# Kernel tuning notes

Measured on AMD Instinct MI355X. Metric: run time of the kernel, lower is better.

The kernel has to match this reference:

```python
import jax, jax.numpy as jnp
import numpy as np

EPS = 1e-5
SLOPE = 0.2  # leaky_relu negative_slope


def _mesh_conv_face(fe, gemm, w, b):
    # fe: [B, C, F]; gemm: [B, F, 3] neighbor face indices; w: [O, C, 4]; b: [O]
    # Gather 3 neighbor faces per face (irregular access).
    nb = jax.vmap(lambda f, g: f[:, g])(fe, gemm)  # [B, C, F, 3]
    n1, n2, n3 = nb[..., 0], nb[..., 1], nb[..., 2]
    # Symmetric (order-invariant) feature columns over the 3 neighbors.
    G = jnp.stack(
        [
            fe,                                                        # center face
            n1 + n2 + n3,                                              # sum
            jnp.abs(n1 - n2) + jnp.abs(n2 - n3) + jnp.abs(n3 - n1),    # pairwise abs-diff sum
            jnp.maximum(n1, jnp.maximum(n2, n3)),                      # max
        ],
        axis=-1,
    )  # [B, C, F, 4]
    # Conv2d with kernel (1,4) == contraction over (C, 4).
    return jnp.einsum('bcfk,ock->bof', G, w) + b[None, :, None]  # [B, O, F]


def _bn(x, gamma, beta):
    # BatchNorm2d (training mode) on [B, C, F]; normalize per-channel over (B, F).
    mu = x.mean(axis=(0, 2), keepdims=True)
    var = x.var(axis=(0, 2), keepdims=True)  # biased, as torch uses for normalization
    xn = (x - mu) * jax.lax.rsqrt(var + EPS)
    return gamma[None, :, None] * xn + beta[None, :, None]


def _lrelu(x):
    return jnp.where(x >= 0, x, SLOPE * x)


def setup_inputs() -> dict:
    key = jax.random.key(0)
    ks = jax.random.split(key, 8)
    B, Cin, Cout, F = 4, 32, 64, 50000
    fe = jax.random.normal(ks[0], (B, Cin, F), dtype=jnp.float32)
    gemm = jax.random.randint(ks[1], (B, F, 3), 0, F)
    w1 = jax.random.normal(ks[2], (Cout, Cin, 4), dtype=jnp.float32) * 0.05
    w2a = jax.random.normal(ks[3], (Cout, Cout, 4), dtype=jnp.float32) * 0.05
    w2b = jax.random.normal(ks[4], (Cout, Cout, 4), dtype=jnp.float32) * 0.05
    z = jnp.zeros((Cout,), jnp.float32)
    o = jnp.ones((Cout,), jnp.float32)
    return {
        'fe': fe, 'gemm': gemm,
        'w1': w1, 'b1': z, 'w2a': w2a, 'b2a': z, 'w2b': w2b, 'b2b': z,
        'g0': o, 'be0': z, 'g1': o, 'be1': z, 'g2': o, 'be2': z,
    }


def reference(fe, gemm, w1, b1, w2a, b2a, w2b, b2b, g0, be0, g1, be1, g2, be2):
    # conv1 -> BN -> LeakyReLU
    x1 = _lrelu(_bn(_mesh_conv_face(fe, gemm, w1, b1), g0, be0))
    # residual block 1
    x2 = _lrelu(_bn(_mesh_conv_face(x1, gemm, w2a, b2a), g1, be1) + x1)
    x1 = x2
    # residual block 2
    x2 = _lrelu(_bn(_mesh_conv_face(x1, gemm, w2b, b2b), g2, be2) + x1)
    return x2  # [B, Cout, F]; pool=0 so before_pool is None
```

## Files before the change

kernel.cpp:

```cpp
#include <hip/hip_runtime.h>
#include <hip/hip_bf16.h>
#include <math.h>


typedef __attribute__((ext_vector_type(8))) short short8;
typedef __attribute__((ext_vector_type(8))) unsigned short ushort8_t;
typedef __attribute__((ext_vector_type(4))) float f32x4;

__device__ inline unsigned short f2bf(float v) {
    union { float f; unsigned u; } x; x.f = v;
    unsigned r = x.u + 0x7fffu + ((x.u >> 16) & 1u);
    return (unsigned short)(r >> 16);
}
__device__ inline float bf2f(unsigned short u) {
    union { unsigned u; float f; } x; x.u = ((unsigned)u) << 16; return x.f;
}
__device__ inline unsigned pk2(float a, float b) {
    union { __hip_bfloat162 h; unsigned u; } c;
    c.h = __float22bfloat162_rn(make_float2(a, b));
    return c.u;
}

__global__ void transpose_fe_kernel(const float* __restrict__ fe,
                                    unsigned short* __restrict__ o, int F)
{
    __shared__ float tile[64 * 33];
    const int b = blockIdx.y;
    const int f0 = blockIdx.x * 64;
    const int t = threadIdx.x;
    const int lane = t & 63;
    const int w = t >> 6;
    const int f = f0 + lane;
    if (f < F) {
#pragma unroll
        for (int i = 0; i < 8; ++i) {
            const int c = w * 8 + i;
            tile[lane * 33 + c] = fe[((size_t)b * 32 + c) * F + f];
        }
    }
    __syncthreads();
    const int j = t >> 2, s = t & 3;
    const int fj = f0 + j;
    if (fj < F) {
        unsigned fw[4];
#pragma unroll
        for (int i = 0; i < 4; ++i)
            fw[i] = pk2(tile[j * 33 + s * 8 + 2 * i], tile[j * 33 + s * 8 + 2 * i + 1]);
        *(uint4*)(o + ((size_t)b * F + fj) * 32 + s * 8) = make_uint4(fw[0], fw[1], fw[2], fw[3]);
    }
}

__global__ void cast_weights_kernel(const float* __restrict__ w1,
                                    const float* __restrict__ w2a,
                                    const float* __restrict__ w2b,
                                    unsigned short* __restrict__ w1b,
                                    unsigned short* __restrict__ w2ab,
                                    unsigned short* __restrict__ w2bb)
{
    const int i = blockIdx.x * blockDim.x + threadIdx.x;
    if (i < 64 * 128) w1b[i] = f2bf(w1[i]);
    if (i < 64 * 256) { w2ab[i] = f2bf(w2a[i]); w2bb[i] = f2bf(w2b[i]); }
}

template <int CIN, bool NORM>
__launch_bounds__(256, (CIN == 32) ? 4 : 2)
__global__ void conv_mfma_kernel(const unsigned short* __restrict__ x,
                                 const int*   __restrict__ gidx,
                                 const unsigned short* __restrict__ wb,
                                 const float* __restrict__ bias,
                                 const float* __restrict__ mrIn,
                                 unsigned short* __restrict__ y,
                                 float* __restrict__ pS,
                                 float* __restrict__ pQ,
                                 int nb, int nbx, int F)
{
    constexpr int NSEG = CIN / 32;
    constexpr int K    = 4 * CIN;
    constexpr int RB   = 2 * K;
    constexpr int GB   = 64 * RB;
    constexpr int GREG = (GB > 17408) ? GB : 17408;
    __shared__ __align__(16) unsigned char smem[GREG + GB];
    float* tile = (float*)smem;
    unsigned char* Wb = smem + GREG;

    const int NBg = gridDim.x;
    const int t = threadIdx.x;
    const int j = t >> 2, s = t & 3;
    const int lane = t & 63, wv = t >> 6;
    const int l15 = lane & 15, quad = lane >> 4;
    const int kb = quad * 8;

    unsigned char* grow = smem + j * RB;
    const int swz = (j & 7) << 4;
    const int nrowi = wv * 16 + l15;
    const unsigned char* nrow = smem + nrowi * RB;
    const int nswz = (nrowi & 7) << 4;

#pragma unroll
    for (int u = 0; u < RB / 64; ++u) {
        const int qb = (s * (RB / 64) + u) * 16;
        const ushort8_t v = *(const ushort8_t*)(wb + (size_t)j * K + qb / 2);
        *(ushort8_t*)(Wb + j * RB + (qb ^ swz)) = v;
    }
    f32x4 bias4[4];
#pragma unroll
    for (int mt = 0; mt < 4; ++mt)
        bias4[mt] = *(const f32x4*)(bias + mt * 16 + quad * 4);

    float scr[NSEG * 8], shr[NSEG * 8];
    if constexpr (NORM) {
#pragma unroll
        for (int i = 0; i < NSEG; ++i) {
            const int c0 = (i * 4 + s) * 8;
#pragma unroll
            for (int h = 0; h < 2; ++h) {
                const f32x4 a  = *(const f32x4*)(mrIn + c0 + 4 * h);
                const f32x4 sh = *(const f32x4*)(mrIn + 64 + c0 + 4 * h);
#pragma unroll
                for (int q = 0; q < 4; ++q) {
                    scr[i * 8 + 4 * h + q] = a[q];
                    shr[i * 8 + 4 * h + q] = sh[q];
                }
            }
        }
    }

    ushort8_t vc[NSEG], v0[NSEG], v1[NSEG], v2[NSEG];
    int gA0, gA1, gA2;
    float S_acc = 0.f, Q_acc = 0.f;
    const int so = t & 63, sg = t >> 6;

    int tl = blockIdx.x;

    {
        const int b0 = tl / nbx;
        const int f0 = (tl - b0 * nbx) * 64;
        const int fc = min(f0 + j, F - 1);
        const int* gp = gidx + ((size_t)b0 * F + fc) * 3;
        const int g0 = gp[0], g1 = gp[1], g2 = gp[2];
        const unsigned short* xb = x + (size_t)b0 * F * CIN;
        const unsigned short* pc = xb + (size_t)fc * CIN;
        const unsigned short* p0 = xb + (size_t)g0 * CIN;
        const unsigned short* p1 = xb + (size_t)g1 * CIN;
        const unsigned short* p2 = xb + (size_t)g2 * CIN;
#pragma unroll
        for (int i = 0; i < NSEG; ++i) {
            const int c0 = (i * 4 + s) * 8;
            vc[i] = *(const ushort8_t*)(pc + c0);
            v0[i] = *(const ushort8_t*)(p0 + c0);
            v1[i] = *(const ushort8_t*)(p1 + c0);
            v2[i] = *(const ushort8_t*)(p2 + c0);
        }
    }
    {
        const int tn = min(tl + NBg, nb - 1);
        const int bn = tn / nbx;
        const int fn = min((tn - bn * nbx) * 64 + j, F - 1);
        const int* gp = gidx + ((size_t)bn * F + fn) * 3;
        gA0 = gp[0]; gA1 = gp[1]; gA2 = gp[2];
    }

    for (; tl < nb; tl += NBg) {
        const int b  = tl / nbx;
        const int f0 = (tl - b * nbx) * 64;

#pragma unroll
        for (int i = 0; i < NSEG; ++i) {
            const int c0 = (i * 4 + s) * 8;
            unsigned fw[16];
#pragma unroll
            for (int q = 0; q < 8; ++q) {
                float ctr = bf2f(vc[i][q]);
                float a   = bf2f(v0[i][q]);
                float bb  = bf2f(v1[i][q]);
                float cc  = bf2f(v2[i][q]);
                if constexpr (NORM) {
                    const float sc_ = scr[i * 8 + q], sh_ = shr[i * 8 + q];
                    ctr = fmaf(ctr, sc_, sh_); ctr = fmaxf(ctr, 0.2f * ctr);
                    a   = fmaf(a,   sc_, sh_); a   = fmaxf(a,   0.2f * a);
                    bb  = fmaf(bb,  sc_, sh_); bb  = fmaxf(bb,  0.2f * bb);
                    cc  = fmaf(cc,  sc_, sh_); cc  = fmaxf(cc,  0.2f * cc);
                }
                const float su = a + bb + cc;
                const float dd = fabsf(a - bb) + fabsf(bb - cc) + fabsf(cc - a);
                const float mm = fmaxf(a, fmaxf(bb, cc));
                fw[2 * q]     = pk2(ctr, su);
                fw[2 * q + 1] = pk2(dd, mm);
            }
#pragma unroll
            for (int q4 = 0; q4 < 4; ++q4) {
                const int qb = 8 * c0 + 16 * q4;
                *(uint4*)(grow + (qb ^ swz)) =
                    make_uint4(fw[4 * q4], fw[4 * q4 + 1], fw[4 * q4 + 2], fw[4 * q4 + 3]);
            }
        }

        {
            const int tn = min(tl + NBg, nb - 1);
            const int bn = tn / nbx;
            const int fcn = min((tn - bn * nbx) * 64 + j, F - 1);
            const unsigned short* xb = x + (size_t)bn * F * CIN;
            const unsigned short* pc = xb + (size_t)fcn * CIN;
            const unsigned short* p0 = xb + (size_t)gA0 * CIN;
            const unsigned short* p1 = xb + (size_t)gA1 * CIN;
            const unsigned short* p2 = xb + (size_t)gA2 * CIN;
#pragma unroll
            for (int i = 0; i < NSEG; ++i) {
                const int c0 = (i * 4 + s) * 8;
                vc[i] = *(const ushort8_t*)(pc + c0);
                v0[i] = *(const ushort8_t*)(p0 + c0);
                v1[i] = *(const ushort8_t*)(p1 + c0);
                v2[i] = *(const ushort8_t*)(p2 + c0);
            }
            const int t2 = min(tl + 2 * NBg, nb - 1);
            const int b2 = t2 / nbx;
            const int f2 = min((t2 - b2 * nbx) * 64 + j, F - 1);
            const int* gp = gidx + ((size_t)b2 * F + f2) * 3;
            gA0 = gp[0]; gA1 = gp[1]; gA2 = gp[2];
        }
        __syncthreads();

        f32x4 acc[4];
#pragma unroll
        for (int mt = 0; mt < 4; ++mt) acc[mt] = (f32x4){0.f, 0.f, 0.f, 0.f};
#pragma unroll
        for (int ks = 0; ks < K; ks += 32) {
            const int cb = 2 * (ks + kb);
            const short8 bfr = *(const short8*)(nrow + (cb ^ nswz));
#pragma unroll
            for (int mt = 0; mt < 4; ++mt) {
                const int ar = mt * 16 + l15;
                const short8 afr = *(const short8*)(Wb + ar * RB + (cb ^ ((ar & 7) << 4)));
                acc[mt] = __builtin_amdgcn_mfma_f32_16x16x32_bf16(afr, bfr, acc[mt], 0, 0, 0);
            }
        }
        __syncthreads();

        {
            const int face = wv * 16 + l15;
#pragma unroll
            for (int mt = 0; mt < 4; ++mt) {
                const int ob = mt * 16 + quad * 4;
                *(f32x4*)(tile + face * 68 + ob) = acc[mt] + bias4[mt];
            }
        }
        __syncthreads();
        {
#pragma unroll
            for (int i = 0; i < 16; ++i) {
                const int f = sg + 4 * i;
                if (f0 + f < F) {
                    const float v = tile[f * 68 + so];
                    S_acc += v; Q_acc += v * v;
                }
            }
        }
        {
            const int f = f0 + j;
            if (f < F) {
                unsigned fw[8];
#pragma unroll
                for (int ii = 0; ii < 8; ++ii)
                    fw[ii] = pk2(tile[j * 68 + s * 16 + 2 * ii],
                                 tile[j * 68 + s * 16 + 2 * ii + 1]);
                unsigned short* yp = y + ((size_t)b * F + f) * 64 + s * 16;
                *(uint4*)yp       = make_uint4(fw[0], fw[1], fw[2], fw[3]);
                *(uint4*)(yp + 8) = make_uint4(fw[4], fw[5], fw[6], fw[7]);
            }
        }
        __syncthreads();
    }

    float* redS = (float*)smem;
    float* redQ = redS + 256;
    redS[t] = S_acc; redQ[t] = Q_acc;
    __syncthreads();
    if (t < 64) {
        pS[(size_t)blockIdx.x * 64 + t] = redS[t] + redS[64 + t] + redS[128 + t] + redS[192 + t];
        pQ[(size_t)blockIdx.x * 64 + t] = redQ[t] + redQ[64 + t] + redQ[128 + t] + redQ[192 + t];
    }
}

__global__ void finalize_kernel(const float* __restrict__ pS, const float* __restrict__ pQ,
                                int nbg, float invN,
                                const float* __restrict__ gamma,
                                const float* __restrict__ beta,
                                float* __restrict__ mr)
{
    __shared__ float rs_[256], rq_[256];
    const int o = blockIdx.x, t = threadIdx.x;
    float S = 0.f, Q = 0.f;
    for (int jj = t; jj < nbg; jj += 256) {
        S += pS[(size_t)jj * 64 + o];
        Q += pQ[(size_t)jj * 64 + o];
    }
    rs_[t] = S; rq_[t] = Q;
    __syncthreads();
#pragma unroll
    for (int s = 128; s > 0; s >>= 1) {
        if (t < s) { rs_[t] += rs_[t + s]; rq_[t] += rq_[t + s]; }
        __syncthreads();
    }
    if (t == 0) {
        const float mu  = rs_[0] * invN;
        const float var = rq_[0] * invN - mu * mu;
        const float rsg = rsqrtf(var + 1e-5f);
        const float sc  = gamma[o] * rsg;
        mr[o]      = sc;
        mr[64 + o] = fmaf(-sc, mu, beta[o]);
    }
}

__global__ void norm_res_kernel(const unsigned short* __restrict__ y1,
                                const unsigned short* __restrict__ y2,
                                const float* __restrict__ mr1,
                                const float* __restrict__ mr2,
                                unsigned short* __restrict__ out,
                                int N8)
{
    const int tid = blockIdx.x * blockDim.x + threadIdx.x;
    if (tid >= N8) return;
    const int c0 = (tid & 7) * 8;
    const ushort8_t a = *(const ushort8_t*)(y1 + (size_t)tid * 8);
    const ushort8_t b = *(const ushort8_t*)(y2 + (size_t)tid * 8);
    float r[8];
#pragma unroll
    for (int h = 0; h < 2; ++h) {
        const f32x4 s1 = *(const f32x4*)(mr1 + c0 + 4 * h);
        const f32x4 h1 = *(const f32x4*)(mr1 + 64 + c0 + 4 * h);
        const f32x4 s2 = *(const f32x4*)(mr2 + c0 + 4 * h);
        const f32x4 h2 = *(const f32x4*)(mr2 + 64 + c0 + 4 * h);
#pragma unroll
        for (int i = 0; i < 4; ++i) {
            float x1 = fmaf(bf2f(a[4 * h + i]), s1[i], h1[i]);
            x1 = fmaxf(x1, 0.2f * x1);
            float v = fmaf(bf2f(b[4 * h + i]), s2[i], h2[i]) + x1;
            r[4 * h + i] = fmaxf(v, 0.2f * v);
        }
    }
    unsigned fw[4];
#pragma unroll
    for (int i = 0; i < 4; ++i) fw[i] = pk2(r[2 * i], r[2 * i + 1]);
    *(uint4*)(out + (size_t)tid * 8) = make_uint4(fw[0], fw[1], fw[2], fw[3]);
}

__global__ void norm_transpose_kernel(const unsigned short* __restrict__ y,
                                      const unsigned short* __restrict__ res,
                                      const float* __restrict__ mr,
                                      float* __restrict__ out, int F)
{
    __shared__ float tile[64 * 65];
    const int b = blockIdx.y, f0 = blockIdx.x * 64, t = threadIdx.x;
    const int j = t >> 2, s = t & 3;
    const int f = f0 + j;
    if (f < F) {
        const size_t row = ((size_t)b * F + f) * 64;
#pragma unroll
        for (int i = 0; i < 2; ++i) {
            const int c0 = s * 16 + i * 8;
            const ushort8_t yv = *(const ushort8_t*)(y + row + c0);
            const ushort8_t rv = *(const ushort8_t*)(res + row + c0);
#pragma unroll
            for (int h = 0; h < 2; ++h) {
                const f32x4 sc = *(const f32x4*)(mr + c0 + 4 * h);
                const f32x4 sh = *(const f32x4*)(mr + 64 + c0 + 4 * h);
#pragma unroll
                for (int q = 0; q < 4; ++q) {
                    float vv = fmaf(bf2f(yv[4 * h + q]), sc[q], sh[q]) + bf2f(rv[4 * h + q]);
                    vv = fmaxf(vv, 0.2f * vv);
                    tile[(c0 + 4 * h + q) * 65 + j] = vv;
                }
            }
        }
    }
    __syncthreads();
    const int o = t >> 2;
    float* ob = out + ((size_t)b * 64 + o) * F + f0;
#pragma unroll
    for (int i = 0; i < 4; ++i) {
        const int fs = (i * 4 + s) * 4;
        if (f0 + fs < F) {
            f32x4 v;
#pragma unroll
            for (int q = 0; q < 4; ++q) v[q] = tile[o * 65 + fs + q];
            *(f32x4*)(ob + fs) = v;
        }
    }
}

extern "C" void kernel_launch(void* const* d_in, const int* in_sizes, int n_in,
                              void* d_out, int out_size, void* d_ws, size_t ws_size,
                              hipStream_t stream)
{
    const float* fe  = (const float*)d_in[0];
    const int*   gm  = (const int*)d_in[1];
    const float* w1  = (const float*)d_in[2];
    const float* b1  = (const float*)d_in[3];
    const float* w2a = (const float*)d_in[4];
    const float* b2a = (const float*)d_in[5];
    const float* w2b = (const float*)d_in[6];
    const float* b2b = (const float*)d_in[7];
    const float* g0  = (const float*)d_in[8];
    const float* be0 = (const float*)d_in[9];
    const float* g1  = (const float*)d_in[10];
    const float* be1 = (const float*)d_in[11];
    const float* g2  = (const float*)d_in[12];
    const float* be2 = (const float*)d_in[13];

    const int B = 4, O = 64;
    const int F = in_sizes[0] / (B * 32);
    const int M = B * F;
    const float invN = 1.0f / (float)M;
    const int nbx = (F + 63) / 64;
    const int nb  = nbx * B;

    unsigned short* Y1 = (unsigned short*)d_ws;
    unsigned short* Y2 = Y1 + (size_t)M * O;
    unsigned short* x2 = Y2 + (size_t)M * O;
    float* pS  = (float*)(x2 + (size_t)M * O);
    float* pQ  = pS + 1024 * 64;
    float* mr1 = pQ + 1024 * 64;
    float* mr2 = mr1 + 128;
    float* mr3 = mr2 + 128;
    unsigned short* w1b  = (unsigned short*)(mr3 + 128);
    unsigned short* w2ab = w1b + 64 * 128;
    unsigned short* w2bb = w2ab + 64 * 256;
    unsigned short* fe_t = (unsigned short*)d_out;

    dim3 blk(256);
    dim3 tgrid(nbx, B);
    const int N8 = M * 8;
    dim3 ngrid((N8 + 255) / 256);
    const int g32 = (nb < 1024) ? nb : 1024;
    const int g64 = (nb < 512)  ? nb : 512;

    transpose_fe_kernel<<<tgrid, blk, 0, stream>>>(fe, fe_t, F);
    cast_weights_kernel<<<64, 256, 0, stream>>>(w1, w2a, w2b, w1b, w2ab, w2bb);

    conv_mfma_kernel<32, false><<<g32, blk, 0, stream>>>(
        fe_t, gm, w1b, b1, nullptr, Y1, pS, pQ, nb, nbx, F);
    finalize_kernel<<<64, 256, 0, stream>>>(pS, pQ, g32, invN, g0, be0, mr1);

    conv_mfma_kernel<64, true><<<g64, blk, 0, stream>>>(
        Y1, gm, w2ab, b2a, mr1, Y2, pS, pQ, nb, nbx, F);
    finalize_kernel<<<64, 256, 0, stream>>>(pS, pQ, g64, invN, g1, be1, mr2);

    norm_res_kernel<<<ngrid, blk, 0, stream>>>(Y1, Y2, mr1, mr2, x2, N8);

    conv_mfma_kernel<64, false><<<g64, blk, 0, stream>>>(
        x2, gm, w2bb, b2b, nullptr, Y1, pS, pQ, nb, nbx, F);
    finalize_kernel<<<64, 256, 0, stream>>>(pS, pQ, g64, invN, g2, be2, mr3);

    norm_transpose_kernel<<<tgrid, blk, 0, stream>>>(Y1, x2, mr3, (float*)d_out, F);
}
```

Baseline: 226.8 us.

## Keep conv weights in registers, drop LDS weight tile, raise occupancy and grids

The conv kernel stops staging the bf16 weight matrix in shared memory. Each wave now holds its 16-output-channel slice of the weights as MFMA A fragments in registers, and the MFMA loop reads only the gathered face tile from LDS. This shrinks the LDS footprint, so launch bounds and grid sizes are raised for higher occupancy, and the partial-sum buffers are enlarged to match the larger grids. The weight cast is folded into the transpose kernel to save one launch. In exchange, register pressure grows, especially for CIN=64 where each thread holds 8 short8 fragments.

Result: faster. 219.7 us (-3.1%).

```diff
diff --git a/kernel.cpp b/kernel.cpp
--- a/kernel.cpp
+++ b/kernel.cpp
@@ -22,12 +22,26 @@
 }
 
 __global__ void transpose_fe_kernel(const float* __restrict__ fe,
-                                    unsigned short* __restrict__ o, int F)
+                                    unsigned short* __restrict__ o, int F,
+                                    const float* __restrict__ w1,
+                                    const float* __restrict__ w2a,
+                                    const float* __restrict__ w2b,
+                                    unsigned short* __restrict__ w1b,
+                                    unsigned short* __restrict__ w2ab,
+                                    unsigned short* __restrict__ w2bb)
 {
     __shared__ float tile[64 * 33];
     const int b = blockIdx.y;
     const int f0 = blockIdx.x * 64;
     const int t = threadIdx.x;
+
+    {
+        const int bid = blockIdx.y * gridDim.x + blockIdx.x;
+        if (bid < 32)       { const int i = bid * 256 + t;        w1b[i]  = f2bf(w1[i]);  }
+        else if (bid < 96)  { const int i = (bid - 32) * 256 + t; w2ab[i] = f2bf(w2a[i]); }
+        else if (bid < 160) { const int i = (bid - 96) * 256 + t; w2bb[i] = f2bf(w2b[i]); }
+    }
+
     const int lane = t & 63;
     const int w = t >> 6;
     const int f = f0 + lane;
@@ -50,20 +64,8 @@
     }
 }
 
-__global__ void cast_weights_kernel(const float* __restrict__ w1,
-                                    const float* __restrict__ w2a,
-                                    const float* __restrict__ w2b,
-                                    unsigned short* __restrict__ w1b,
-                                    unsigned short* __restrict__ w2ab,
-                                    unsigned short* __restrict__ w2bb)
-{
-    const int i = blockIdx.x * blockDim.x + threadIdx.x;
-    if (i < 64 * 128) w1b[i] = f2bf(w1[i]);
-    if (i < 64 * 256) { w2ab[i] = f2bf(w2a[i]); w2bb[i] = f2bf(w2b[i]); }
-}
-
 template <int CIN, bool NORM>
-__launch_bounds__(256, (CIN == 32) ? 4 : 2)
+__launch_bounds__(256, (CIN == 32) ? 5 : (NORM ? 3 : 4))
 __global__ void conv_mfma_kernel(const unsigned short* __restrict__ x,
                                  const int*   __restrict__ gidx,
                                  const unsigned short* __restrict__ wb,
@@ -79,9 +81,8 @@
     constexpr int RB   = 2 * K;
     constexpr int GB   = 64 * RB;
     constexpr int GREG = (GB > 17408) ? GB : 17408;
-    __shared__ __align__(16) unsigned char smem[GREG + GB];
+    __shared__ __align__(16) unsigned char smem[GREG];
     float* tile = (float*)smem;
-    unsigned char* Wb = smem + GREG;
 
     const int NBg = gridDim.x;
     const int t = threadIdx.x;
@@ -92,20 +93,15 @@
 
     unsigned char* grow = smem + j * RB;
     const int swz = (j & 7) << 4;
-    const int nrowi = wv * 16 + l15;
-    const unsigned char* nrow = smem + nrowi * RB;
-    const int nswz = (nrowi & 7) << 4;
-
-#pragma unroll
-    for (int u = 0; u < RB / 64; ++u) {
-        const int qb = (s * (RB / 64) + u) * 16;
-        const ushort8_t v = *(const ushort8_t*)(wb + (size_t)j * K + qb / 2);
-        *(ushort8_t*)(Wb + j * RB + (qb ^ swz)) = v;
-    }
-    f32x4 bias4[4];
-#pragma unroll
-    for (int mt = 0; mt < 4; ++mt)
-        bias4[mt] = *(const f32x4*)(bias + mt * 16 + quad * 4);
+
+    short8 afr[K / 32];
+    {
+        const int ar = wv * 16 + l15;
+#pragma unroll
+        for (int ksi = 0; ksi < K / 32; ++ksi)
+            afr[ksi] = *(const short8*)(wb + (size_t)ar * K + ksi * 32 + kb);
+    }
+    const f32x4 bias4 = *(const f32x4*)(bias + wv * 16 + quad * 4);
 
     float scr[NSEG * 8], shr[NSEG * 8];
     if constexpr (NORM) {
@@ -222,26 +218,25 @@
 
         f32x4 acc[4];
 #pragma unroll
-        for (int mt = 0; mt < 4; ++mt) acc[mt] = (f32x4){0.f, 0.f, 0.f, 0.f};
-#pragma unroll
-        for (int ks = 0; ks < K; ks += 32) {
-            const int cb = 2 * (ks + kb);
-            const short8 bfr = *(const short8*)(nrow + (cb ^ nswz));
-#pragma unroll
-            for (int mt = 0; mt < 4; ++mt) {
-                const int ar = mt * 16 + l15;
-                const short8 afr = *(const short8*)(Wb + ar * RB + (cb ^ ((ar & 7) << 4)));
-                acc[mt] = __builtin_amdgcn_mfma_f32_16x16x32_bf16(afr, bfr, acc[mt], 0, 0, 0);
+        for (int nt = 0; nt < 4; ++nt) acc[nt] = (f32x4){0.f, 0.f, 0.f, 0.f};
+#pragma unroll
+        for (int ksi = 0; ksi < K / 32; ++ksi) {
+            const int cb = 2 * (ksi * 32 + kb);
+#pragma unroll
+            for (int nt = 0; nt < 4; ++nt) {
+                const int nr = nt * 16 + l15;
+                const short8 bfr = *(const short8*)(smem + nr * RB + (cb ^ ((nr & 7) << 4)));
+                acc[nt] = __builtin_amdgcn_mfma_f32_16x16x32_bf16(afr[ksi], bfr, acc[nt], 0, 0, 0);
             }
         }
         __syncthreads();
 
         {
-            const int face = wv * 16 + l15;
-#pragma unroll
-            for (int mt = 0; mt < 4; ++mt) {
-                const int ob = mt * 16 + quad * 4;
-                *(f32x4*)(tile + face * 68 + ob) = acc[mt] + bias4[mt];
+            const int cb0 = wv * 16 + quad * 4;
+#pragma unroll
+            for (int nt = 0; nt < 4; ++nt) {
+                const int face = nt * 16 + l15;
+                *(f32x4*)(tile + face * 68 + cb0) = acc[nt] + bias4;
             }
         }
         __syncthreads();
@@ -418,8 +413,8 @@
     unsigned short* Y2 = Y1 + (size_t)M * O;
     unsigned short* x2 = Y2 + (size_t)M * O;
     float* pS  = (float*)(x2 + (size_t)M * O);
-    float* pQ  = pS + 1024 * 64;
-    float* mr1 = pQ + 1024 * 64;
+    float* pQ  = pS + 2048 * 64;
+    float* mr1 = pQ + 2048 * 64;
     float* mr2 = mr1 + 128;
     float* mr3 = mr2 + 128;
     unsigned short* w1b  = (unsigned short*)(mr3 + 128);
@@ -431,25 +426,26 @@
     dim3 tgrid(nbx, B);
     const int N8 = M * 8;
     dim3 ngrid((N8 + 255) / 256);
-    const int g32 = (nb < 1024) ? nb : 1024;
-    const int g64 = (nb < 512)  ? nb : 512;
-
-    transpose_fe_kernel<<<tgrid, blk, 0, stream>>>(fe, fe_t, F);
-    cast_weights_kernel<<<64, 256, 0, stream>>>(w1, w2a, w2b, w1b, w2ab, w2bb);
-
-    conv_mfma_kernel<32, false><<<g32, blk, 0, stream>>>(
+    const int g1g = (nb < 1280) ? nb : 1280;
+    const int g2g = (nb < 768)  ? nb : 768;
+    const int g3g = (nb < 1024) ? nb : 1024;
+
+    transpose_fe_kernel<<<tgrid, blk, 0, stream>>>(fe, fe_t, F,
+                                                   w1, w2a, w2b, w1b, w2ab, w2bb);
+
+    conv_mfma_kernel<32, false><<<g1g, blk, 0, stream>>>(
         fe_t, gm, w1b, b1, nullptr, Y1, pS, pQ, nb, nbx, F);
-    finalize_kernel<<<64, 256, 0, stream>>>(pS, pQ, g32, invN, g0, be0, mr1);
-
-    conv_mfma_kernel<64, true><<<g64, blk, 0, stream>>>(
+    finalize_kernel<<<64, 256, 0, stream>>>(pS, pQ, g1g, invN, g0, be0, mr1);
+
+    conv_mfma_kernel<64, true><<<g2g, blk, 0, stream>>>(
         Y1, gm, w2ab, b2a, mr1, Y2, pS, pQ, nb, nbx, F);
-    finalize_kernel<<<64, 256, 0, stream>>>(pS, pQ, g64, invN, g1, be1, mr2);
+    finalize_kernel<<<64, 256, 0, stream>>>(pS, pQ, g2g, invN, g1, be1, mr2);
 
     norm_res_kernel<<<ngrid, blk, 0, stream>>>(Y1, Y2, mr1, mr2, x2, N8);
 
-    conv_mfma_kernel<64, false><<<g64, blk, 0, stream>>>(
+    conv_mfma_kernel<64, false><<<g3g, blk, 0, stream>>>(
         x2, gm, w2bb, b2b, nullptr, Y1, pS, pQ, nb, nbx, F);
-    finalize_kernel<<<64, 256, 0, stream>>>(pS, pQ, g64, invN, g2, be2, mr3);
+    finalize_kernel<<<64, 256, 0, stream>>>(pS, pQ, g3g, invN, g2, be2, mr3);
 
     norm_transpose_kernel<<<tgrid, blk, 0, stream>>>(Y1, x2, mr3, (float*)d_out, F);
 }
```
